# Optimization experiments

Hardware: AMD Instinct MI355X
Metric: run time of the kernel (lower is better)

The kernel has to match this reference:

```python
import jax, jax.numpy as jnp
import numpy as np


def setup_inputs() -> dict:
    key = jax.random.key(0)
    k1, k2 = jax.random.split(key)
    N, M, C = 8192, 16384, 128
    features = jax.random.normal(k1, (N, 1, 1, C), dtype=jnp.float32)
    patch_memory = jax.random.normal(k2, (1, M, 1, C), dtype=jnp.float32)
    return {"features": features, "patch_memory": patch_memory}


def reference(features, patch_memory):
    # Faithful to: torch.norm(features - patch_memory, dim=3); torch.min(dim=1)
    # features: [N, 1, 1, C], patch_memory: [1, M, 1, C] -> broadcast diff [N, M, 1, C]
    # Avoid materializing the [N, M, C] diff tensor: use the GEMM expansion
    # ||a-b||^2 = ||a||^2 + ||b||^2 - 2 a.b (same math, efficient form).
    f = features.reshape(features.shape[0], features.shape[-1])       # [N, C]
    m = patch_memory.reshape(patch_memory.shape[1], patch_memory.shape[-1])  # [M, C]
    f2 = jnp.sum(f * f, axis=-1)   # [N]
    m2 = jnp.sum(m * m, axis=-1)   # [M]
    cross = jnp.einsum('nc,mc->nm', f, m)  # [N, M]
    d2 = f2[:, None] + m2[None, :] - 2.0 * cross
    distances = jnp.sqrt(jnp.maximum(d2, 0.0))       # [N, M] == norm over dim 3
    min_distances = jnp.min(distances, axis=1)       # min over memory dim (dim=1)
    # original keeps the trailing singleton patch dim -> [N, 1]
    return min_distances[:, None]
```

## Files before the change

kernel.cpp:

```cpp
#include <hip/hip_runtime.h>
#include <hip/hip_bf16.h>
#include <stdint.h>

#define N_ROWS 8192
#define M_ROWS 16384
#define CDIM 128
#define MSPLIT 16
#define SLICE_ROWS 1024
#define NT 32

typedef unsigned short u16;
typedef __attribute__((ext_vector_type(8))) short bf16x8;
typedef __attribute__((ext_vector_type(16))) float f32x16;

static __device__ __forceinline__ u16 f2bf(float x) {
  union { float f; uint32_t u; } v; v.f = x;
  uint32_t u = v.u;
  uint32_t r = u + 0x7FFFu + ((u >> 16) & 1u);
  return (u16)(r >> 16);
}
static __device__ __forceinline__ float bf2f(u16 b) {
  union { uint32_t u; float f; } v; v.u = ((uint32_t)b) << 16;
  return v.f;
}

__global__ __launch_bounds__(256) void prep_kernel(
    const float* __restrict__ f, const float* __restrict__ m,
    u16* __restrict__ fb, u16* __restrict__ mb,
    float* __restrict__ f2, float* __restrict__ mh, int* __restrict__ mind2)
{
  const int row = blockIdx.x * 4 + (threadIdx.x >> 6);
  const int lane = threadIdx.x & 63;
  const bool isF = row < N_ROWS;
  const int r = isF ? row : row - N_ROWS;
  const float* src = (isF ? f : m) + (size_t)r * CDIM;
  float2 v = *(const float2*)(src + lane * 2);
  u16 b0 = f2bf(v.x), b1 = f2bf(v.y);
  float x0 = bf2f(b0), x1 = bf2f(b1);
  float s = x0 * x0 + x1 * x1;
#pragma unroll
  for (int mask = 1; mask < 64; mask <<= 1)
    s += __shfl_xor(s, mask, 64);

  const int t = r >> 5, lr = r & 31;
  const int ks = lane >> 3;
  const int l5p = (lane >> 2) & 1;
  const int j = (lane & 3) * 2;
  u16* dst = (isF ? fb : mb)
             + ((size_t)(t * 8 + ks) * 64 + l5p * 32 + lr) * 8 + j;
  dst[0] = b0; dst[1] = b1;
  if (lane == 0) {
    if (isF) { f2[r] = s; mind2[r] = 0x7F7FFFFF; }
    else     { mh[r] = -0.5f * s; }
  }
}

__global__ __launch_bounds__(256, 2) void gemm_min_kernel(
    const u16* __restrict__ fb, const u16* __restrict__ mb,
    const float* __restrict__ f2, const float* __restrict__ mh,
    int* __restrict__ mind2)
{
  const int tid = threadIdx.x;
  const int lane = tid & 63;
  const int w = tid >> 6;
  const int l31 = lane & 31;
  const int l5 = lane >> 5;
  const int abase = blockIdx.y * 256;
  const size_t mslice = (size_t)blockIdx.x * SLICE_ROWS;

  bf16x8 af[2][8];
#pragma unroll
  for (int mi = 0; mi < 2; ++mi) {
    const int ta = (abase >> 5) + w * 2 + mi;
#pragma unroll
    for (int ks = 0; ks < 8; ++ks)
      af[mi][ks] = *(const bf16x8*)&fb[((size_t)(ta * 8 + ks) * 64 + lane) * 8];
  }

  const u16* bbase = mb + ((size_t)(mslice >> 5) * 8 * 64) * 8;
  const float* mhp = mh + mslice + l31;

  bf16x8 bgA[8], bgB[8];
  float mhA, mhB;
#pragma unroll
  for (int ks = 0; ks < 8; ++ks)
    bgA[ks] = *(const bf16x8*)&bbase[((size_t)ks * 64 + lane) * 8];
  mhA = mhp[0];

  float tmax[2][16];
#pragma unroll
  for (int mi = 0; mi < 2; ++mi)
#pragma unroll
    for (int r = 0; r < 16; ++r) tmax[mi][r] = -3.0e38f;

  f32x16 accA[2], accB[2];
#pragma unroll
  for (int mi = 0; mi < 2; ++mi)
#pragma unroll
    for (int r = 0; r < 16; ++r) accB[mi][r] = -3.0e38f;

  for (int t = 0; t < NT; t += 2) {
    {
      const u16* bp1 = bbase + (size_t)(t + 1) * (8 * 64 * 8);
#pragma unroll
      for (int ks = 0; ks < 8; ++ks)
        bgB[ks] = *(const bf16x8*)&bp1[((size_t)ks * 64 + lane) * 8];
      mhB = mhp[(t + 1) * 32];
    }
#pragma unroll
    for (int mi = 0; mi < 2; ++mi)
#pragma unroll
      for (int r = 0; r < 16; ++r) accA[mi][r] = mhA;
#pragma unroll
    for (int ks = 0; ks < 8; ++ks)
#pragma unroll
      for (int mi = 0; mi < 2; ++mi)
        accA[mi] = __builtin_amdgcn_mfma_f32_32x32x16_bf16(
            af[mi][ks], bgA[ks], accA[mi], 0, 0, 0);
#pragma unroll
    for (int mi = 0; mi < 2; ++mi)
#pragma unroll
      for (int r = 0; r < 16; ++r)
        tmax[mi][r] = fmaxf(tmax[mi][r], accB[mi][r]);

    {
      const u16* bp2 = bbase + (size_t)((t + 2) & (NT - 1)) * (8 * 64 * 8);
#pragma unroll
      for (int ks = 0; ks < 8; ++ks)
        bgA[ks] = *(const bf16x8*)&bp2[((size_t)ks * 64 + lane) * 8];
      mhA = mhp[((t + 2) & (NT - 1)) * 32];
    }
#pragma unroll
    for (int mi = 0; mi < 2; ++mi)
#pragma unroll
      for (int r = 0; r < 16; ++r) accB[mi][r] = mhB;
#pragma unroll
    for (int ks = 0; ks < 8; ++ks)
#pragma unroll
      for (int mi = 0; mi < 2; ++mi)
        accB[mi] = __builtin_amdgcn_mfma_f32_32x32x16_bf16(
            af[mi][ks], bgB[ks], accB[mi], 0, 0, 0);
#pragma unroll
    for (int mi = 0; mi < 2; ++mi)
#pragma unroll
      for (int r = 0; r < 16; ++r)
        tmax[mi][r] = fmaxf(tmax[mi][r], accA[mi][r]);
  }
#pragma unroll
  for (int mi = 0; mi < 2; ++mi)
#pragma unroll
    for (int r = 0; r < 16; ++r)
      tmax[mi][r] = fmaxf(tmax[mi][r], accB[mi][r]);

#pragma unroll
  for (int mi = 0; mi < 2; ++mi)
#pragma unroll
    for (int r = 0; r < 16; ++r) {
      float tv = tmax[mi][r];
      tv = fmaxf(tv, __shfl_xor(tv, 1, 64));
      tv = fmaxf(tv, __shfl_xor(tv, 2, 64));
      tv = fmaxf(tv, __shfl_xor(tv, 4, 64));
      tv = fmaxf(tv, __shfl_xor(tv, 8, 64));
      tv = fmaxf(tv, __shfl_xor(tv, 16, 64));
      tmax[mi][r] = tv;
    }
  if (l31 == 0) {
#pragma unroll
    for (int mi = 0; mi < 2; ++mi)
#pragma unroll
      for (int r = 0; r < 16; ++r) {
        const int row = abase + w * 64 + mi * 32
                        + (r & 3) + 8 * (r >> 2) + 4 * l5;
        const float d2 = fmaxf(fmaf(-2.0f, tmax[mi][r], f2[row]), 0.0f);
        atomicMin(&mind2[row], __float_as_int(d2));
      }
  }
}

__global__ __launch_bounds__(256) void finalize_kernel(
    const int* __restrict__ mind2, float* __restrict__ out)
{
  const int i = blockIdx.x * 256 + threadIdx.x;
  out[i] = sqrtf(fmaxf(__int_as_float(mind2[i]), 0.0f));
}

extern "C" void kernel_launch(void* const* d_in, const int* in_sizes, int n_in,
                              void* d_out, int out_size, void* d_ws, size_t ws_size,
                              hipStream_t stream) {
  const float* f = (const float*)d_in[0];
  const float* m = (const float*)d_in[1];

  char* ws = (char*)d_ws;
  u16*  fb    = (u16*)(ws);
  u16*  mb    = (u16*)(ws + (2u << 20));
  float* f2   = (float*)(ws + (2u << 20) + (4u << 20));
  float* mh   = (float*)(ws + (2u << 20) + (4u << 20) + (32u << 10));
  int*  mind2 = (int*)(ws + (2u << 20) + (4u << 20) + (96u << 10));

  hipLaunchKernelGGL(prep_kernel, dim3((N_ROWS + M_ROWS) / 4), dim3(256), 0, stream,
                     f, m, fb, mb, f2, mh, mind2);
  hipLaunchKernelGGL(gemm_min_kernel, dim3(MSPLIT, N_ROWS / 256), dim3(256), 0, stream,
                     fb, mb, f2, mh, mind2);
  hipLaunchKernelGGL(finalize_kernel, dim3(N_ROWS / 256), dim3(256), 0, stream,
                     mind2, (float*)d_out);
}
```

Baseline: 55.66 us.

## Stage memory-bank tiles in LDS via async global_load_lds triple buffering

The GEMM-min kernel now uses 512-thread blocks (2x4 waves) that share B tiles of 128 memory rows. Each tile is loaded once per block into a triple-buffered LDS ring with global_load_lds, instead of every wave streaming its own B fragments from global memory. The grid is reshaped to 4 M-splits by 64 row blocks, and MFMA sections are wrapped in s_setprio. The aim is to cut redundant global and L2 traffic for B, in exchange for per-tile barriers, LDS read traffic and fewer, larger blocks.

```diff
diff --git a/kernel.cpp b/kernel.cpp
--- a/kernel.cpp
+++ b/kernel.cpp
@@ -5,9 +5,10 @@
 #define N_ROWS 8192
 #define M_ROWS 16384
 #define CDIM 128
-#define MSPLIT 16
-#define SLICE_ROWS 1024
+#define MSPLIT 4
 #define NT 32
+#define BTR 128
+#define TILE_U16 (BTR * CDIM)
 
 typedef unsigned short u16;
 typedef __attribute__((ext_vector_type(8))) short bf16x8;
@@ -23,6 +24,11 @@
   union { uint32_t u; float f; } v; v.u = ((uint32_t)b) << 16;
   return v.f;
 }
+
+#define GLOAD_LDS(gsrc, ldst)                                                  \
+  __builtin_amdgcn_global_load_lds(                                            \
+      (const __attribute__((address_space(1))) uint32_t*)(gsrc),               \
+      (__attribute__((address_space(3))) uint32_t*)(ldst), 16, 0, 0)
 
 __global__ __launch_bounds__(256) void prep_kernel(
     const float* __restrict__ f, const float* __restrict__ m,
@@ -55,37 +61,49 @@
   }
 }
 
-__global__ __launch_bounds__(256, 2) void gemm_min_kernel(
+__global__ __launch_bounds__(512, 2) void gemm_min_kernel(
     const u16* __restrict__ fb, const u16* __restrict__ mb,
     const float* __restrict__ f2, const float* __restrict__ mh,
     int* __restrict__ mind2)
 {
+  __shared__ __align__(16) u16 bts[3 * TILE_U16];
+  __shared__ __align__(16) float mhl[4096];
   const int tid = threadIdx.x;
   const int lane = tid & 63;
   const int w = tid >> 6;
+  const int wm = w >> 2;
+  const int wn = w & 3;
   const int l31 = lane & 31;
   const int l5 = lane >> 5;
-  const int abase = blockIdx.y * 256;
-  const size_t mslice = (size_t)blockIdx.x * SLICE_ROWS;
+  const int abase = blockIdx.y * 128;
+  const size_t mslice = (size_t)blockIdx.x * 4096;
 
   bf16x8 af[2][8];
 #pragma unroll
   for (int mi = 0; mi < 2; ++mi) {
-    const int ta = (abase >> 5) + w * 2 + mi;
+    const int ta = (abase >> 5) + wm * 2 + mi;
 #pragma unroll
     for (int ks = 0; ks < 8; ++ks)
       af[mi][ks] = *(const bf16x8*)&fb[((size_t)(ta * 8 + ks) * 64 + lane) * 8];
   }
 
-  const u16* bbase = mb + ((size_t)(mslice >> 5) * 8 * 64) * 8;
-  const float* mhp = mh + mslice + l31;
-
-  bf16x8 bgA[8], bgB[8];
-  float mhA, mhB;
-#pragma unroll
-  for (int ks = 0; ks < 8; ++ks)
-    bgA[ks] = *(const bf16x8*)&bbase[((size_t)ks * 64 + lane) * 8];
-  mhA = mhp[0];
+  const float* mhsrc = mh + mslice;
+#pragma unroll
+  for (int c = 0; c < 2; ++c) {
+    const int c16 = c * 512 + tid;
+    GLOAD_LDS(mhsrc + c16 * 4, mhl + c16 * 4);
+  }
+  const u16* mbase_ptr = mb + mslice * CDIM;
+#pragma unroll
+  for (int tt = 0; tt < 2; ++tt)
+#pragma unroll
+    for (int c = 0; c < 4; ++c) {
+      const int t16 = c * 512 + tid;
+      GLOAD_LDS(mbase_ptr + (size_t)tt * TILE_U16 + t16 * 8,
+                bts + tt * TILE_U16 + t16 * 8);
+    }
+  asm volatile("s_waitcnt vmcnt(4)" ::: "memory");
+  __builtin_amdgcn_s_barrier();
 
   float tmax[2][16];
 #pragma unroll
@@ -99,52 +117,89 @@
 #pragma unroll
     for (int r = 0; r < 16; ++r) accB[mi][r] = -3.0e38f;
 
+  const int wnoff = wn * (8 * 64 * 8);
+  int c0 = 0;
+
   for (int t = 0; t < NT; t += 2) {
+    int c1 = c0 + 1; if (c1 >= 3) c1 -= 3;
+    int c2 = c0 + 2; if (c2 >= 3) c2 -= 3;
+
     {
-      const u16* bp1 = bbase + (size_t)(t + 1) * (8 * 64 * 8);
-#pragma unroll
-      for (int ks = 0; ks < 8; ++ks)
-        bgB[ks] = *(const bf16x8*)&bp1[((size_t)ks * 64 + lane) * 8];
-      mhB = mhp[(t + 1) * 32];
-    }
-#pragma unroll
-    for (int mi = 0; mi < 2; ++mi)
-#pragma unroll
-      for (int r = 0; r < 16; ++r) accA[mi][r] = mhA;
-#pragma unroll
-    for (int ks = 0; ks < 8; ++ks)
-#pragma unroll
-      for (int mi = 0; mi < 2; ++mi)
-        accA[mi] = __builtin_amdgcn_mfma_f32_32x32x16_bf16(
-            af[mi][ks], bgA[ks], accA[mi], 0, 0, 0);
-#pragma unroll
-    for (int mi = 0; mi < 2; ++mi)
-#pragma unroll
-      for (int r = 0; r < 16; ++r)
-        tmax[mi][r] = fmaxf(tmax[mi][r], accB[mi][r]);
+      const u16* bt = bts + c0 * TILE_U16 + wnoff;
+      bf16x8 bg[8];
+#pragma unroll
+      for (int ks = 0; ks < 8; ++ks)
+        bg[ks] = *(const bf16x8*)&bt[((size_t)ks * 64 + lane) * 8];
+      const float mhA = mhl[t * BTR + wn * 32 + l31];
+      {
+        const u16* srcT = mbase_ptr + (size_t)((t + 2) & (NT - 1)) * TILE_U16;
+        u16* dstT = bts + c2 * TILE_U16;
+#pragma unroll
+        for (int c = 0; c < 4; ++c) {
+          const int t16 = c * 512 + tid;
+          GLOAD_LDS(srcT + t16 * 8, dstT + t16 * 8);
+        }
+      }
+      asm volatile("s_waitcnt vmcnt(4)" ::: "memory");
+      __builtin_amdgcn_s_barrier();
+
+#pragma unroll
+      for (int mi = 0; mi < 2; ++mi)
+#pragma unroll
+        for (int r = 0; r < 16; ++r) accA[mi][r] = mhA;
+      __builtin_amdgcn_s_setprio(1);
+#pragma unroll
+      for (int ks = 0; ks < 8; ++ks)
+#pragma unroll
+        for (int mi = 0; mi < 2; ++mi)
+          accA[mi] = __builtin_amdgcn_mfma_f32_32x32x16_bf16(
+              af[mi][ks], bg[ks], accA[mi], 0, 0, 0);
+      __builtin_amdgcn_s_setprio(0);
+#pragma unroll
+      for (int mi = 0; mi < 2; ++mi)
+#pragma unroll
+        for (int r = 0; r < 16; ++r)
+          tmax[mi][r] = fmaxf(tmax[mi][r], accB[mi][r]);
+    }
 
     {
-      const u16* bp2 = bbase + (size_t)((t + 2) & (NT - 1)) * (8 * 64 * 8);
-#pragma unroll
-      for (int ks = 0; ks < 8; ++ks)
-        bgA[ks] = *(const bf16x8*)&bp2[((size_t)ks * 64 + lane) * 8];
-      mhA = mhp[((t + 2) & (NT - 1)) * 32];
-    }
-#pragma unroll
-    for (int mi = 0; mi < 2; ++mi)
-#pragma unroll
-      for (int r = 0; r < 16; ++r) accB[mi][r] = mhB;
-#pragma unroll
-    for (int ks = 0; ks < 8; ++ks)
-#pragma unroll
-      for (int mi = 0; mi < 2; ++mi)
-        accB[mi] = __builtin_amdgcn_mfma_f32_32x32x16_bf16(
-            af[mi][ks], bgB[ks], accB[mi], 0, 0, 0);
-#pragma unroll
-    for (int mi = 0; mi < 2; ++mi)
-#pragma unroll
-      for (int r = 0; r < 16; ++r)
-        tmax[mi][r] = fmaxf(tmax[mi][r], accA[mi][r]);
+      const u16* bt = bts + c1 * TILE_U16 + wnoff;
+      bf16x8 bg[8];
+#pragma unroll
+      for (int ks = 0; ks < 8; ++ks)
+        bg[ks] = *(const bf16x8*)&bt[((size_t)ks * 64 + lane) * 8];
+      const float mhB = mhl[(t + 1) * BTR + wn * 32 + l31];
+      {
+        const u16* srcT = mbase_ptr + (size_t)((t + 3) & (NT - 1)) * TILE_U16;
+        u16* dstT = bts + c0 * TILE_U16;
+#pragma unroll
+        for (int c = 0; c < 4; ++c) {
+          const int t16 = c * 512 + tid;
+          GLOAD_LDS(srcT + t16 * 8, dstT + t16 * 8);
+        }
+      }
+      asm volatile("s_waitcnt vmcnt(4)" ::: "memory");
+      __builtin_amdgcn_s_barrier();
+
+#pragma unroll
+      for (int mi = 0; mi < 2; ++mi)
+#pragma unroll
+        for (int r = 0; r < 16; ++r) accB[mi][r] = mhB;
+      __builtin_amdgcn_s_setprio(1);
+#pragma unroll
+      for (int ks = 0; ks < 8; ++ks)
+#pragma unroll
+        for (int mi = 0; mi < 2; ++mi)
+          accB[mi] = __builtin_amdgcn_mfma_f32_32x32x16_bf16(
+              af[mi][ks], bg[ks], accB[mi], 0, 0, 0);
+      __builtin_amdgcn_s_setprio(0);
+#pragma unroll
+      for (int mi = 0; mi < 2; ++mi)
+#pragma unroll
+        for (int r = 0; r < 16; ++r)
+          tmax[mi][r] = fmaxf(tmax[mi][r], accA[mi][r]);
+    }
+    c0 = c2;
   }
 #pragma unroll
   for (int mi = 0; mi < 2; ++mi)
@@ -169,7 +224,7 @@
     for (int mi = 0; mi < 2; ++mi)
 #pragma unroll
       for (int r = 0; r < 16; ++r) {
-        const int row = abase + w * 64 + mi * 32
+        const int row = abase + wm * 64 + mi * 32
                         + (r & 3) + 8 * (r >> 2) + 4 * l5;
         const float d2 = fmaxf(fmaf(-2.0f, tmax[mi][r], f2[row]), 0.0f);
         atomicMin(&mind2[row], __float_as_int(d2));
@@ -199,7 +254,7 @@
 
   hipLaunchKernelGGL(prep_kernel, dim3((N_ROWS + M_ROWS) / 4), dim3(256), 0, stream,
                      f, m, fb, mb, f2, mh, mind2);
-  hipLaunchKernelGGL(gemm_min_kernel, dim3(MSPLIT, N_ROWS / 256), dim3(256), 0, stream,
+  hipLaunchKernelGGL(gemm_min_kernel, dim3(MSPLIT, N_ROWS / 128), dim3(512), 0, stream,
                      fb, mb, f2, mh, mind2);
   hipLaunchKernelGGL(finalize_kernel, dim3(N_ROWS / 256), dim3(256), 0, stream,
                      mind2, (float*)d_out);
```

After: 52.31 us. -6.0%, faster.
